# Optimization experiments

Measured on AMD Instinct MI355X. Metric: run time of the kernel, lower is better.

## Reference

```python
import jax, jax.numpy as jnp
import numpy as np

DOT_THRESHOLD = 0.9995  # fall back to normalized lerp when quats nearly parallel
EPS = 1e-8


def _normalize(q, axis=-1):
    return q / jnp.clip(jnp.linalg.norm(q, axis=axis, keepdims=True), 1e-12)


def _quaternion_slerp(q0, q1, t):
    """Batched slerp. q0,q1: (N,4); t: (N,). Standard shortest-arc slerp."""
    dot = jnp.sum(q0 * q1, axis=-1)
    q1 = jnp.where(dot[..., None] < 0.0, -q1, q1)  # take shortest path
    dot = jnp.clip(jnp.abs(dot), -1.0, 1.0)
    theta = jnp.arccos(dot)
    sin_theta = jnp.sin(theta)
    safe_sin = jnp.where(sin_theta < EPS, 1.0, sin_theta)
    s0 = jnp.sin((1.0 - t) * theta) / safe_sin
    s1 = jnp.sin(t * theta) / safe_sin
    slerped = s0[..., None] * q0 + s1[..., None] * q1
    # near-parallel fallback: normalized linear interpolation
    lerped = _normalize(q0 + t[..., None] * (q1 - q0))
    return jnp.where(dot[..., None] > DOT_THRESHOLD, lerped, slerped)


def setup_inputs() -> dict:
    key = jax.random.key(0)
    k1, k2, k3 = jax.random.split(key, 3)
    N = 8_388_608  # number of time samples
    K = 64         # num_keyframes
    t = jax.random.uniform(k1, (N,), dtype=jnp.float32)
    translations = jax.random.normal(k2, (K, 3), dtype=jnp.float32) * 0.1
    quaternions = jax.random.normal(k3, (K, 4), dtype=jnp.float32)
    quaternions = quaternions.at[:, 0].add(2.0)  # bias toward identity like init
    keyframe_times = jnp.linspace(0.0, 1.0, K, dtype=jnp.float32)
    return {"t": t, "translations": translations, "quaternions": quaternions,
            "keyframe_times": keyframe_times}


def reference(t, translations, quaternions, keyframe_times):
    quats = _normalize(quaternions)  # F.normalize(self.quaternions, dim=-1)
    K = keyframe_times.shape[0]
    orig_shape = t.shape
    tf = t.reshape(-1)  # (N,)

    idx = jnp.searchsorted(keyframe_times, tf)  # left, matches torch default
    idx = jnp.clip(idx, 1, K - 1)
    idx_prev = idx - 1

    t_prev = keyframe_times[idx_prev]
    t_next = keyframe_times[idx]
    local_t = (tf - t_prev) / (t_next - t_prev + 1e-8)  # (N,)

    trans_prev = translations[idx_prev]  # (N,3)
    trans_next = translations[idx]
    quat_prev = quats[idx_prev]          # (N,4)
    quat_next = quats[idx]

    trans = (1.0 - local_t)[..., None] * trans_prev + local_t[..., None] * trans_next
    quat = _quaternion_slerp(quat_prev, quat_next, local_t)

    return trans.reshape(*orig_shape, 3), quat.reshape(*orig_shape, 4)
```

## Files before the change

kernel.cpp:

```cpp
#include <hip/hip_runtime.h>
#include <math.h>


#define KFR   64
#define NSEG  63
#define BLOCK 256
#define CHUNK 1024

__global__ __launch_bounds__(BLOCK) void temporal_motor_kernel(
    const float* __restrict__ t_in,
    const float* __restrict__ translations,
    const float* __restrict__ quaternions,
    const float* __restrict__ keyframe_times,
    float* __restrict__ out_trans,
    float* __restrict__ out_quat,
    int nchunks)
{
    __shared__ float4 sA[KFR];
    __shared__ float4 sB[KFR];
    __shared__ float4 sC[KFR];
    __shared__ float4 sQ0[KFR];
    __shared__ float4 sQ1[KFR];

    const int tid = threadIdx.x;
    if (tid < NSEG) {
        const int s = tid;
        float t0 = keyframe_times[s];
        float t1 = keyframe_times[s + 1];

        float ax = quaternions[4 * s + 0], ay = quaternions[4 * s + 1];
        float az = quaternions[4 * s + 2], aw = quaternions[4 * s + 3];
        float bx = quaternions[4 * s + 4], by = quaternions[4 * s + 5];
        float bz = quaternions[4 * s + 6], bw = quaternions[4 * s + 7];
        float ia = 1.0f / fmaxf(sqrtf(ax * ax + ay * ay + az * az + aw * aw), 1e-12f);
        float ib = 1.0f / fmaxf(sqrtf(bx * bx + by * by + bz * bz + bw * bw), 1e-12f);
        ax *= ia; ay *= ia; az *= ia; aw *= ia;
        bx *= ib; by *= ib; bz *= ib; bw *= ib;

        float d0 = ax * bx + ay * by + az * bz + aw * bw;
        float sgn = (d0 < 0.0f) ? -1.0f : 1.0f;
        bx *= sgn; by *= sgn; bz *= sgn; bw *= sgn;
        float d = fminf(fabsf(d0), 1.0f);

        float theta = acosf(d);
        float st    = sqrtf(fmaxf(1.0f - d * d, 0.0f));
        float inv_st = (d > 0.9995f) ? 0.0f : (1.0f / st);

        float px = translations[3 * s + 0], py = translations[3 * s + 1];
        float pz = translations[3 * s + 2];
        float nx = translations[3 * s + 3], ny = translations[3 * s + 4];
        float nz = translations[3 * s + 5];

        sA[s]  = make_float4(t0, t1, 1.0f / (t1 - t0 + 1e-8f), theta);
        sB[s]  = make_float4(px, py, pz, inv_st);
        sC[s]  = make_float4(nx - px, ny - py, nz - pz, d);
        sQ0[s] = make_float4(ax, ay, az, aw);
        sQ1[s] = make_float4(bx, by, bz, bw);
    }
    __syncthreads();

    const int lane = tid & 63;
    const int wave = tid >> 6;

    for (int chunk = blockIdx.x; chunk < nchunks; chunk += gridDim.x) {
        const int base = chunk * CHUNK + wave * 256 + lane;

        #pragma unroll
        for (int j = 0; j < 4; ++j) {
            const int idx = base + j * 64;
            const float tt = t_in[idx];

            int s = (int)ceilf(tt * (float)NSEG) - 1;
            s = (s < 0) ? 0 : (s > NSEG - 1) ? NSEG - 1 : s;
            float4 a = sA[s];
            while (s > 0 && a.x >= tt)        { --s; a = sA[s]; }
            while (s < NSEG - 1 && a.y < tt)  { ++s; a = sA[s]; }

            const float lt  = (tt - a.x) * a.z;
            const float omt = 1.0f - lt;

            const float4 b = sB[s];
            const float4 c = sC[s];

            float3 tr;
            tr.x = fmaf(lt, c.x, b.x);
            tr.y = fmaf(lt, c.y, b.y);
            tr.z = fmaf(lt, c.z, b.z);

            float sn, cs;
            __sincosf(lt * a.w, &sn, &cs);
            const float d   = c.w;
            const float wbs = sn * b.w;
            const float was = cs - d * wbs;

            const float s2  = fmaf(-2.0f * lt * omt, 1.0f - d, 1.0f);
            const float inv = rsqrtf(fmaxf(s2, 1e-24f));
            const float wal = omt * inv;
            const float wbl = lt * inv;

            const bool fb = (d > 0.9995f);
            const float wa = fb ? wal : was;
            const float wb = fb ? wbl : wbs;

            const float4 q0 = sQ0[s];
            const float4 q1 = sQ1[s];
            float4 oq;
            oq.x = wa * q0.x + wb * q1.x;
            oq.y = wa * q0.y + wb * q1.y;
            oq.z = wa * q0.z + wb * q1.z;
            oq.w = wa * q0.w + wb * q1.w;

            *(float3*)(out_trans + (size_t)idx * 3) = tr;
            *(float4*)(out_quat  + (size_t)idx * 4) = oq;
        }
    }
}

__global__ void temporal_motor_tail(
    const float* __restrict__ t_in,
    const float* __restrict__ translations,
    const float* __restrict__ quaternions,
    const float* __restrict__ keyframe_times,
    float* __restrict__ out_trans,
    float* __restrict__ out_quat,
    int n_start, int n, int K)
{
    int i = n_start + blockIdx.x * blockDim.x + threadIdx.x;
    if (i >= n) return;
    float tt = t_in[i];

    int g = 1;
    while (g < K - 1 && keyframe_times[g] < tt) ++g;
    float tpw = keyframe_times[g - 1], tnw = keyframe_times[g];
    float lt = (tt - tpw) / (tnw - tpw + 1e-8f);
    float omt = 1.0f - lt;

    for (int c = 0; c < 3; ++c)
        out_trans[3 * (size_t)i + c] =
            omt * translations[3 * (g - 1) + c] + lt * translations[3 * g + c];

    float q0[4], q1[4];
    float n0 = 0, n1 = 0;
    for (int c = 0; c < 4; ++c) { q0[c] = quaternions[4 * (g - 1) + c]; n0 += q0[c] * q0[c]; }
    for (int c = 0; c < 4; ++c) { q1[c] = quaternions[4 * g + c];       n1 += q1[c] * q1[c]; }
    float i0 = 1.0f / fmaxf(sqrtf(n0), 1e-12f), i1 = 1.0f / fmaxf(sqrtf(n1), 1e-12f);
    float d = 0;
    for (int c = 0; c < 4; ++c) { q0[c] *= i0; q1[c] *= i1; }
    for (int c = 0; c < 4; ++c) d += q0[c] * q1[c];
    float sgn = (d < 0.0f) ? -1.0f : 1.0f;
    for (int c = 0; c < 4; ++c) q1[c] *= sgn;
    d = fminf(fabsf(d), 1.0f);
    float theta = acosf(d);
    float st = sqrtf(fmaxf(1.0f - d * d, 0.0f));
    float invst = (st < 1e-8f) ? 1.0f : (1.0f / st);
    float s0 = __sinf(omt * theta) * invst, s1 = __sinf(lt * theta) * invst;
    float l[4], ln = 0;
    for (int c = 0; c < 4; ++c) { l[c] = q0[c] + lt * (q1[c] - q0[c]); ln += l[c] * l[c]; }
    float li = 1.0f / fmaxf(sqrtf(ln), 1e-12f);
    bool fb = (d > 0.9995f);
    for (int c = 0; c < 4; ++c)
        out_quat[4 * (size_t)i + c] = fb ? l[c] * li : (s0 * q0[c] + s1 * q1[c]);
}

extern "C" void kernel_launch(void* const* d_in, const int* in_sizes, int n_in,
                              void* d_out, int out_size, void* d_ws, size_t ws_size,
                              hipStream_t stream) {
    const float* t_in  = (const float*)d_in[0];
    const float* trans = (const float*)d_in[1];
    const float* quats = (const float*)d_in[2];
    const float* ktime = (const float*)d_in[3];
    const int N = in_sizes[0];
    const int K = in_sizes[3];

    float* out_trans = (float*)d_out;
    float* out_quat  = (float*)d_out + (size_t)N * 3;

    if (K == KFR) {
        const int nchunks = N / CHUNK;
        if (nchunks > 0) {
            int blocks = nchunks < 2048 ? nchunks : 2048;
            temporal_motor_kernel<<<blocks, BLOCK, 0, stream>>>(
                t_in, trans, quats, ktime, out_trans, out_quat, nchunks);
        }
        const int rem_start = nchunks * CHUNK;
        if (rem_start < N) {
            int rem = N - rem_start;
            temporal_motor_tail<<<(rem + 63) / 64, 64, 0, stream>>>(
                t_in, trans, quats, ktime, out_trans, out_quat, rem_start, N, K);
        }
    } else {
        temporal_motor_tail<<<(N + 255) / 256, 256, 0, stream>>>(
            t_in, trans, quats, ktime, out_trans, out_quat, 0, N, K);
    }
}
```

Before: 262.4 us.

## Pack keyframe tables as fp16, stage translations through LDS, use nontemporal I/O

Keyframe segment data (translations, deltas, quaternions, theta, 1-d) is packed as half2 pairs into fewer shared-memory float4 tables, which cuts LDS reads per sample. Translation outputs are staged per wave in shared memory so each wave can write them as coalesced 16-byte vector stores instead of 12-byte stores. Input loads and output stores use nontemporal hints. The fp16 packing lowers the precision of quaternions and translations, which risks tolerance failures. There is also no wave barrier between the staging write and the read, which could be a correctness hazard.

```diff
diff --git a/kernel.cpp b/kernel.cpp
--- a/kernel.cpp
+++ b/kernel.cpp
@@ -1,4 +1,5 @@
 #include <hip/hip_runtime.h>
+#include <hip/hip_fp16.h>
 #include <math.h>
 
 
@@ -6,6 +7,21 @@
 #define NSEG  63
 #define BLOCK 256
 #define CHUNK 1024
+
+typedef float v4f __attribute__((ext_vector_type(4)));
+
+static __device__ __forceinline__ float pack2h(float a, float b) {
+    __half2 h = __floats2half2_rn(a, b);
+    unsigned int u;
+    __builtin_memcpy(&u, &h, 4);
+    return __uint_as_float(u);
+}
+static __device__ __forceinline__ float2 unpack2h(float p) {
+    unsigned int u = __float_as_uint(p);
+    __half2 h;
+    __builtin_memcpy(&h, &u, 4);
+    return __half22float2(h);
+}
 
 __global__ __launch_bounds__(BLOCK) void temporal_motor_kernel(
     const float* __restrict__ t_in,
@@ -17,10 +33,9 @@
     int nchunks)
 {
     __shared__ float4 sA[KFR];
-    __shared__ float4 sB[KFR];
-    __shared__ float4 sC[KFR];
-    __shared__ float4 sQ0[KFR];
-    __shared__ float4 sQ1[KFR];
+    __shared__ float4 sT[KFR];
+    __shared__ float4 sQ[KFR];
+    __shared__ __align__(16) float sStage[BLOCK / 64][192];
 
     const int tid = threadIdx.x;
     if (tid < NSEG) {
@@ -42,25 +57,25 @@
         bx *= sgn; by *= sgn; bz *= sgn; bw *= sgn;
         float d = fminf(fabsf(d0), 1.0f);
 
-        float theta = acosf(d);
-        float st    = sqrtf(fmaxf(1.0f - d * d, 0.0f));
+        float theta  = acosf(d);
+        float st     = sqrtf(fmaxf(1.0f - d * d, 0.0f));
         float inv_st = (d > 0.9995f) ? 0.0f : (1.0f / st);
 
         float px = translations[3 * s + 0], py = translations[3 * s + 1];
         float pz = translations[3 * s + 2];
-        float nx = translations[3 * s + 3], ny = translations[3 * s + 4];
-        float nz = translations[3 * s + 5];
-
-        sA[s]  = make_float4(t0, t1, 1.0f / (t1 - t0 + 1e-8f), theta);
-        sB[s]  = make_float4(px, py, pz, inv_st);
-        sC[s]  = make_float4(nx - px, ny - py, nz - pz, d);
-        sQ0[s] = make_float4(ax, ay, az, aw);
-        sQ1[s] = make_float4(bx, by, bz, bw);
+        float dx = translations[3 * s + 3] - px;
+        float dy = translations[3 * s + 4] - py;
+        float dz = translations[3 * s + 5] - pz;
+
+        sA[s] = make_float4(t0, t1, 1.0f / (t1 - t0 + 1e-8f), pack2h(theta, 1.0f - d));
+        sT[s] = make_float4(pack2h(px, py), pack2h(pz, dx), pack2h(dy, dz), inv_st);
+        sQ[s] = make_float4(pack2h(ax, ay), pack2h(az, aw), pack2h(bx, by), pack2h(bz, bw));
     }
     __syncthreads();
 
     const int lane = tid & 63;
     const int wave = tid >> 6;
+    float* stg = sStage[wave];
 
     for (int chunk = blockIdx.x; chunk < nchunks; chunk += gridDim.x) {
         const int base = chunk * CHUNK + wave * 256 + lane;
@@ -68,7 +83,7 @@
         #pragma unroll
         for (int j = 0; j < 4; ++j) {
             const int idx = base + j * 64;
-            const float tt = t_in[idx];
+            const float tt = __builtin_nontemporal_load(t_in + idx);
 
             int s = (int)ceilf(tt * (float)NSEG) - 1;
             s = (s < 0) ? 0 : (s > NSEG - 1) ? NSEG - 1 : s;
@@ -78,40 +93,45 @@
 
             const float lt  = (tt - a.x) * a.z;
             const float omt = 1.0f - lt;
-
-            const float4 b = sB[s];
-            const float4 c = sC[s];
-
-            float3 tr;
-            tr.x = fmaf(lt, c.x, b.x);
-            tr.y = fmaf(lt, c.y, b.y);
-            tr.z = fmaf(lt, c.z, b.z);
+            const float2 thd = unpack2h(a.w);
+
+            const float4 tv   = sT[s];
+            const float2 pxy  = unpack2h(tv.x);
+            const float2 pzdx = unpack2h(tv.y);
+            const float2 dydz = unpack2h(tv.z);
+            const float inv_st = tv.w;
 
             float sn, cs;
-            __sincosf(lt * a.w, &sn, &cs);
-            const float d   = c.w;
-            const float wbs = sn * b.w;
-            const float was = cs - d * wbs;
-
-            const float s2  = fmaf(-2.0f * lt * omt, 1.0f - d, 1.0f);
+            __sincosf(lt * thd.x, &sn, &cs);
+            const float wbs = sn * inv_st;
+            const float was = fmaf(thd.y, wbs, cs - wbs);
+
+            const float s2  = fmaf(-2.0f * lt * omt, thd.y, 1.0f);
             const float inv = rsqrtf(fmaxf(s2, 1e-24f));
-            const float wal = omt * inv;
-            const float wbl = lt * inv;
-
-            const bool fb = (d > 0.9995f);
-            const float wa = fb ? wal : was;
-            const float wb = fb ? wbl : wbs;
-
-            const float4 q0 = sQ0[s];
-            const float4 q1 = sQ1[s];
-            float4 oq;
-            oq.x = wa * q0.x + wb * q1.x;
-            oq.y = wa * q0.y + wb * q1.y;
-            oq.z = wa * q0.z + wb * q1.z;
-            oq.w = wa * q0.w + wb * q1.w;
-
-            *(float3*)(out_trans + (size_t)idx * 3) = tr;
-            *(float4*)(out_quat  + (size_t)idx * 4) = oq;
+            const bool  fb  = (inv_st == 0.0f);
+            const float wa  = fb ? omt * inv : was;
+            const float wb  = fb ? lt * inv  : wbs;
+
+            const float4 qv  = sQ[s];
+            const float2 q0a = unpack2h(qv.x), q0b = unpack2h(qv.y);
+            const float2 q1a = unpack2h(qv.z), q1b = unpack2h(qv.w);
+            v4f oq;
+            oq.x = wa * q0a.x + wb * q1a.x;
+            oq.y = wa * q0a.y + wb * q1a.y;
+            oq.z = wa * q0b.x + wb * q1b.x;
+            oq.w = wa * q0b.y + wb * q1b.y;
+
+            stg[lane * 3 + 0] = fmaf(lt, pzdx.y, pxy.x);
+            stg[lane * 3 + 1] = fmaf(lt, dydz.x, pxy.y);
+            stg[lane * 3 + 2] = fmaf(lt, dydz.y, pzdx.x);
+
+            __builtin_nontemporal_store(oq, (v4f*)out_quat + idx);
+
+            const int g = idx - lane;
+            if (lane < 48) {
+                v4f v = ((v4f*)stg)[lane];
+                __builtin_nontemporal_store(v, (v4f*)(out_trans + (size_t)g * 3) + lane);
+            }
         }
     }
 }
@@ -175,7 +195,7 @@
     float* out_trans = (float*)d_out;
     float* out_quat  = (float*)d_out + (size_t)N * 3;
 
-    if (K == KFR) {
+    if (K == KFR && (N & 3) == 0) {
         const int nchunks = N / CHUNK;
         if (nchunks > 0) {
             int blocks = nchunks < 2048 ? nchunks : 2048;
```

New measurement: 266.2 us. About the same (+1.5%).
